# Kernel optimization log

Measured on AMD Instinct MI355X. Metric: run time of the kernel, lower is better.

## Reference

```python
import jax, jax.numpy as jnp
import numpy as np

BIN_SIZE = 128  # bin_size init arg

def elu(x):
    return jnp.where(x > 0, x, jnp.expm1(x))

def setup_inputs() -> dict:
    key = jax.random.key(0)
    ks = jax.random.split(key, 8)
    B, N, D, F = 2, 6400, 32, 256
    x_dist = jax.random.normal(ks[0], (B, N, D), jnp.float32)
    x_features = jax.random.normal(ks[1], (B, N, F), jnp.float32)
    msk = jax.random.randint(ks[2], (B, N), 0, 2) > 0
    codebook = jax.random.normal(ks[3], (D, 100), jnp.float32)  # (distance_dim, max_num_bins//2)
    W1 = jax.random.normal(ks[4], (2 * D, 32), jnp.float32) * (1.0 / np.sqrt(2 * D)).astype(np.float32)
    b1 = jnp.zeros((32,), jnp.float32)
    W2 = jax.random.normal(ks[5], (32, 32), jnp.float32) * np.float32(1.0 / np.sqrt(32))
    b2 = jnp.zeros((32,), jnp.float32)
    W3 = jax.random.normal(ks[6], (32, 32), jnp.float32) * np.float32(1.0 / np.sqrt(32))
    b3 = jnp.zeros((32,), jnp.float32)
    return dict(x_dist=x_dist, x_features=x_features, msk=msk, codebook=codebook,
                W1=W1, b1=b1, W2=W2, b2=b2, W3=W3, b3=b3)

def reference(x_dist, x_features, msk, codebook, W1, b1, W2, b2, W3, b3):
    B, N, D = x_dist.shape
    n_bins = N // BIN_SIZE
    # LSH projections: [B,N,n_bins//2] -> mirrored to [B,N,n_bins]
    mul = jnp.einsum('bnd,dh->bnh', x_dist, codebook[:, :n_bins // 2])
    cmul = jnp.concatenate([mul, -mul], axis=-1)
    # masked-out points are pushed into the last bin
    bin_idx = jnp.argmax(cmul, axis=-1) + jnp.where(~msk, n_bins - 1, 0)
    bins_split = jnp.argsort(bin_idx, axis=-1).reshape(B, n_bins, BIN_SIZE)  # [B,nb,bs]
    gather = jax.vmap(lambda x, i: x[i])  # batched gather over axis 1
    x_dist_binned = gather(x_dist, bins_split)          # [B,nb,bs,D]
    x_features_binned = gather(x_features, bins_split)  # [B,nb,bs,F]
    msk_f = msk.astype(x_dist.dtype)[..., None]         # [B,N,1]
    msk_f_binned = gather(msk_f, bins_split)            # [B,nb,bs,1]
    # pairwise learnable kernel: concat(a_i, b_j) -> 3-layer FFN -> elu
    a = jnp.broadcast_to(x_dist_binned[:, :, :, None, :], (B, n_bins, BIN_SIZE, BIN_SIZE, D))
    b = jnp.broadcast_to(x_dist_binned[:, :, None, :, :], (B, n_bins, BIN_SIZE, BIN_SIZE, D))
    res = jnp.concatenate([a, b], axis=-1)              # [B,nb,bs,bs,2D]
    h = elu(res @ W1 + b1)
    h = elu(h @ W2 + b2)
    dm = elu(h @ W3 + b3)                               # [B,nb,bs,bs,32]
    m = msk_f_binned[..., 0]                            # [B,nb,bs]
    dm = dm * m[:, :, :, None, None] * m[:, :, None, :, None]
    return (bins_split, x_features_binned, dm, msk_f_binned)
```

## Files before the change

kernel.cpp:

```cpp
#include <hip/hip_runtime.h>

#define BATCH 2
#define NPT 6400
#define DD 32
#define FF 256
#define BS 128
#define NBINS 50
#define NHALF 25
#define NPTS (BATCH * NPT)
#define NKEY 100
#define IST 8

typedef __bf16 bf16x8 __attribute__((ext_vector_type(8)));
typedef float f32x4 __attribute__((ext_vector_type(4)));

__device__ __forceinline__ float elu_f(float x) {
    return x > 0.0f ? x : (__expf(x) - 1.0f);
}

__global__ void k_binkey(const float* __restrict__ xd, const float* __restrict__ cb,
                         const int* __restrict__ msk, int* __restrict__ keys) {
    int g = blockIdx.x * blockDim.x + threadIdx.x;
    if (g >= NPTS) return;
    const float* xr = xd + (size_t)g * DD;
    float x[DD];
#pragma unroll
    for (int d = 0; d < DD; ++d) x[d] = xr[d];
    float mul[NHALF];
#pragma unroll
    for (int h = 0; h < NHALF; ++h) {
        float s = 0.f;
#pragma unroll
        for (int d = 0; d < DD; ++d) s = fmaf(x[d], cb[d * 100 + h], s);
        mul[h] = s;
    }
    float best = mul[0];
    int bi = 0;
#pragma unroll
    for (int h = 1; h < NHALF; ++h)
        if (mul[h] > best) { best = mul[h]; bi = h; }
#pragma unroll
    for (int h = 0; h < NHALF; ++h) {
        float v = -mul[h];
        if (v > best) { best = v; bi = NHALF + h; }
    }
    keys[g] = bi + (msk[g] != 0 ? 0 : (NBINS - 1));
}

__global__ void k_sort(const int* __restrict__ keys, float* __restrict__ bins_f,
                       int* __restrict__ bins_i) {
    __shared__ unsigned char sk[NPT];
    __shared__ unsigned short lh[NKEY][258];
    __shared__ int base[128];
    int b = blockIdx.x;
    int t = threadIdx.x;
    for (int i = t; i < NPT; i += 256) sk[i] = (unsigned char)keys[b * NPT + i];
    for (int k = 0; k < NKEY; ++k) lh[k][t] = 0;
    __syncthreads();
    const int CH = NPT / 256;
    int i0 = t * CH;
#pragma unroll
    for (int i = 0; i < CH; ++i) lh[sk[i0 + i]][t]++;
    __syncthreads();
    int myrun = 0;
    if (t < NKEY) {
        int run = 0;
        for (int c = 0; c < 256; ++c) {
            int v = lh[t][c];
            lh[t][c] = (unsigned short)run;
            run += v;
        }
        myrun = run;
    }
    if (t < 128) base[t] = myrun;
    __syncthreads();
    for (int off = 1; off < 128; off <<= 1) {
        int v = (t < 128 && t >= off) ? base[t - off] : 0;
        __syncthreads();
        if (t < 128) base[t] += v;
        __syncthreads();
    }
    if (t < 128) base[t] -= myrun;
    __syncthreads();
#pragma unroll
    for (int i = 0; i < CH; ++i) {
        int idx = i0 + i;
        int k = sk[idx];
        int pos = base[k] + lh[k][t];
        lh[k][t] = (unsigned short)(lh[k][t] + 1);
        bins_f[b * NPT + pos] = (float)idx;
        bins_i[b * NPT + pos] = idx;
    }
}

__global__ void k_points(const float* __restrict__ xd, const int* __restrict__ msk,
                         const int* __restrict__ bins_i, const float* __restrict__ W1,
                         const float* __restrict__ b1, float* __restrict__ a1b1,
                         float* __restrict__ mws, float* __restrict__ out_msk) {
    int g = blockIdx.x * blockDim.x + threadIdx.x;
    int p_lin = g >> 5;
    int c = g & 31;
    if (p_lin >= NPTS) return;
    int bb = p_lin / NPT;
    int idx = bins_i[p_lin];
    const float* xr = xd + ((size_t)(bb * NPT + idx)) * DD;
    float a = 0.f, bv = b1[c];
#pragma unroll
    for (int d = 0; d < DD; ++d) {
        float xv = xr[d];
        a = fmaf(xv, W1[d * 32 + c], a);
        bv = fmaf(xv, W1[(DD + d) * 32 + c], bv);
    }
    a1b1[(size_t)p_lin * 64 + c] = a;
    a1b1[(size_t)p_lin * 64 + 32 + c] = bv;
    if (c == 0) {
        float m = (msk[bb * NPT + idx] != 0) ? 1.0f : 0.0f;
        mws[p_lin] = m;
        out_msk[p_lin] = m;
    }
}

__global__ void k_feat(const float* __restrict__ xf, const int* __restrict__ bins_i,
                       float* __restrict__ out_feat) {
    int g = blockIdx.x * blockDim.x + threadIdx.x;
    if (g >= NPTS * (FF / 4)) return;
    int row = g >> 6;
    int q = g & 63;
    int bb = row / NPT;
    int idx = bins_i[row];
    const float4* src = (const float4*)(xf + ((size_t)(bb * NPT + idx)) * FF);
    float4* dst = (float4*)(out_feat + (size_t)row * FF);
    dst[q] = src[q];
}

__global__ void __launch_bounds__(256) k_pairs(
    const float* __restrict__ a1b1, const float* __restrict__ mws,
    const float* __restrict__ W2, const float* __restrict__ b2,
    const float* __restrict__ W3, const float* __restrict__ b3,
    float* __restrict__ out_dm) {
    __shared__ __attribute__((aligned(16))) float B1s[128][36];
    __shared__ __attribute__((aligned(16))) float A1s[IST][36];
    __shared__ float mjs[128];
    __shared__ float mis[IST];
    __shared__ __attribute__((aligned(16))) __bf16 scr[4][2][16 * 40];

    int t = threadIdx.x;
    int lane = t & 63;
    int wv = t >> 6;
    int n = lane & 15;
    int quad = lane >> 4;
    int koct = quad * 8;

    int bin = blockIdx.x >> 4;
    int strip = blockIdx.x & 15;
    int i_base = strip * IST;
    int base_p = bin * 128;

    for (int idx = t; idx < 128 * 8; idx += 256) {
        int r = idx >> 3, q = idx & 7;
        *(float4*)&B1s[r][q * 4] =
            *(const float4*)&a1b1[(size_t)(base_p + r) * 64 + 32 + q * 4];
    }
    if (t < IST * 8) {
        int r = t >> 3, q = t & 7;
        *(float4*)&A1s[r][q * 4] =
            *(const float4*)&a1b1[(size_t)(base_p + i_base + r) * 64 + q * 4];
    }
    if (t < 128) mjs[t] = mws[base_p + t];
    if (t < IST) mis[t] = mws[base_p + i_base + t];

    bf16x8 w2f0, w2f1, w3f0, w3f1;
#pragma unroll
    for (int j = 0; j < 8; ++j) {
        w2f0[j] = (__bf16)W2[(koct + j) * 32 + n];
        w2f1[j] = (__bf16)W2[(koct + j) * 32 + n + 16];
        w3f0[j] = (__bf16)W3[(koct + j) * 32 + n];
        w3f1[j] = (__bf16)W3[(koct + j) * 32 + n + 16];
    }
    float b2lo = b2[n], b2hi = b2[n + 16];
    float b3lo = b3[n], b3hi = b3[n + 16];
    __syncthreads();

    const f32x4 z = {0.f, 0.f, 0.f, 0.f};
    for (int g = 0; g < 16; ++g) {
        int grp = g * 4 + wv;
        int i_l = grp >> 3;
        int j0 = (grp & 7) * 16;

        float aA[8], bB[8];
        *(float4*)&aA[0] = *(float4*)&A1s[i_l][koct];
        *(float4*)&aA[4] = *(float4*)&A1s[i_l][koct + 4];
        *(float4*)&bB[0] = *(float4*)&B1s[j0 + n][koct];
        *(float4*)&bB[4] = *(float4*)&B1s[j0 + n][koct + 4];
        bf16x8 h1;
#pragma unroll
        for (int j = 0; j < 8; ++j) h1[j] = (__bf16)elu_f(aA[j] + bB[j]);

        f32x4 acc0 = __builtin_amdgcn_mfma_f32_16x16x32_bf16(h1, w2f0, z, 0, 0, 0);
        f32x4 acc1 = __builtin_amdgcn_mfma_f32_16x16x32_bf16(h1, w2f1, z, 0, 0, 0);

        __bf16* sc = &scr[wv][g & 1][0];
#pragma unroll
        for (int r = 0; r < 4; ++r) {
            sc[(quad * 4 + r) * 40 + n] = (__bf16)elu_f(acc0[r] + b2lo);
            sc[(quad * 4 + r) * 40 + n + 16] = (__bf16)elu_f(acc1[r] + b2hi);
        }
        __syncthreads();

        bf16x8 h2 = *(bf16x8*)&sc[n * 40 + koct];
        f32x4 acc2 = __builtin_amdgcn_mfma_f32_16x16x32_bf16(h2, w3f0, z, 0, 0, 0);
        f32x4 acc3 = __builtin_amdgcn_mfma_f32_16x16x32_bf16(h2, w3f1, z, 0, 0, 0);

        float miv = mis[i_l];
        size_t obase = ((size_t)(bin * 128 + i_base + i_l) * 128 + j0) * 32;
#pragma unroll
        for (int r = 0; r < 4; ++r) {
            int jr = quad * 4 + r;
            float mm = miv * mjs[j0 + jr];
            out_dm[obase + (size_t)jr * 32 + n] = elu_f(acc2[r] + b3lo) * mm;
            out_dm[obase + (size_t)jr * 32 + n + 16] = elu_f(acc3[r] + b3hi) * mm;
        }
    }
}

extern "C" void kernel_launch(void* const* d_in, const int* in_sizes, int n_in,
                              void* d_out, int out_size, void* d_ws, size_t ws_size,
                              hipStream_t stream) {
    const float* xd  = (const float*)d_in[0];
    const float* xf  = (const float*)d_in[1];
    const int*   msk = (const int*)d_in[2];
    const float* cb  = (const float*)d_in[3];
    const float* W1  = (const float*)d_in[4];
    const float* b1  = (const float*)d_in[5];
    const float* W2  = (const float*)d_in[6];
    const float* b2  = (const float*)d_in[7];
    const float* W3  = (const float*)d_in[8];
    const float* b3  = (const float*)d_in[9];

    float* out = (float*)d_out;
    float* out_bins = out;
    float* out_feat = out + 12800;
    float* out_dm   = out + 12800 + 3276800;
    float* out_msk  = out + 12800 + 3276800 + 52428800;

    int*   keys   = (int*)d_ws;
    int*   bins_i = keys + NPTS;
    float* a1b1   = (float*)(bins_i + NPTS);
    float* mws    = a1b1 + (size_t)NPTS * 64;

    k_binkey<<<NPTS / 256, 256, 0, stream>>>(xd, cb, msk, keys);
    k_sort<<<BATCH, 256, 0, stream>>>(keys, out_bins, bins_i);
    k_points<<<NPTS * 32 / 256, 256, 0, stream>>>(xd, msk, bins_i, W1, b1, a1b1, mws, out_msk);
    k_feat<<<NPTS * 64 / 256, 256, 0, stream>>>(xf, bins_i, out_feat);
    k_pairs<<<100 * 16, 256, 0, stream>>>(a1b1, mws, W2, b2, W3, b3, out_dm);
}
```

Before: 289.9 us.

## Fuse point gather kernels and drop block barrier in pair MLP loop

Merges the W1 projection kernel and the feature gather kernel into one launch, where each wavefront handles one point, copying its feature row and computing both halves of the first-layer projection. In the pair kernel, the per-iteration block-wide __syncthreads is removed and the double-buffered per-wave scratch becomes a single buffer. The scratch is private to each wave, so the barrier was not needed for data sharing. Dropping it relies on lockstep wavefront execution to order the LDS writes before the reads, with no explicit wave-level fence.

```diff
diff --git a/kernel.cpp b/kernel.cpp
--- a/kernel.cpp
+++ b/kernel.cpp
@@ -93,44 +93,39 @@
     }
 }
 
-__global__ void k_points(const float* __restrict__ xd, const int* __restrict__ msk,
-                         const int* __restrict__ bins_i, const float* __restrict__ W1,
-                         const float* __restrict__ b1, float* __restrict__ a1b1,
-                         float* __restrict__ mws, float* __restrict__ out_msk) {
-    int g = blockIdx.x * blockDim.x + threadIdx.x;
-    int p_lin = g >> 5;
-    int c = g & 31;
+__global__ void __launch_bounds__(256) k_gather(
+    const float* __restrict__ xd, const float* __restrict__ xf,
+    const int* __restrict__ msk, const int* __restrict__ bins_i,
+    const float* __restrict__ W1, const float* __restrict__ b1,
+    float* __restrict__ out_feat, float* __restrict__ a1b1,
+    float* __restrict__ mws, float* __restrict__ out_msk) {
+    int t = threadIdx.x;
+    int wv = t >> 6;
+    int l = t & 63;
+    int p_lin = blockIdx.x * 4 + wv;
     if (p_lin >= NPTS) return;
     int bb = p_lin / NPT;
     int idx = bins_i[p_lin];
-    const float* xr = xd + ((size_t)(bb * NPT + idx)) * DD;
-    float a = 0.f, bv = b1[c];
-#pragma unroll
-    for (int d = 0; d < DD; ++d) {
-        float xv = xr[d];
-        a = fmaf(xv, W1[d * 32 + c], a);
-        bv = fmaf(xv, W1[(DD + d) * 32 + c], bv);
-    }
-    a1b1[(size_t)p_lin * 64 + c] = a;
-    a1b1[(size_t)p_lin * 64 + 32 + c] = bv;
-    if (c == 0) {
-        float m = (msk[bb * NPT + idx] != 0) ? 1.0f : 0.0f;
+    int src_row = bb * NPT + idx;
+
+    const float4* src = (const float4*)(xf + (size_t)src_row * FF);
+    float4* dst = (float4*)(out_feat + (size_t)p_lin * FF);
+    dst[l] = src[l];
+
+    const float* xr = xd + (size_t)src_row * DD;
+    int c = l & 31;
+    int side = l >> 5;
+    float acc = side ? b1[c] : 0.f;
+    const float* Wcol = W1 + (size_t)side * DD * 32;
+#pragma unroll
+    for (int d = 0; d < DD; ++d) acc = fmaf(xr[d], Wcol[d * 32 + c], acc);
+    a1b1[(size_t)p_lin * 64 + l] = acc;
+
+    if (l == 0) {
+        float m = (msk[src_row] != 0) ? 1.0f : 0.0f;
         mws[p_lin] = m;
         out_msk[p_lin] = m;
     }
-}
-
-__global__ void k_feat(const float* __restrict__ xf, const int* __restrict__ bins_i,
-                       float* __restrict__ out_feat) {
-    int g = blockIdx.x * blockDim.x + threadIdx.x;
-    if (g >= NPTS * (FF / 4)) return;
-    int row = g >> 6;
-    int q = g & 63;
-    int bb = row / NPT;
-    int idx = bins_i[row];
-    const float4* src = (const float4*)(xf + ((size_t)(bb * NPT + idx)) * FF);
-    float4* dst = (float4*)(out_feat + (size_t)row * FF);
-    dst[q] = src[q];
 }
 
 __global__ void __launch_bounds__(256) k_pairs(
@@ -142,7 +137,7 @@
     __shared__ __attribute__((aligned(16))) float A1s[IST][36];
     __shared__ float mjs[128];
     __shared__ float mis[IST];
-    __shared__ __attribute__((aligned(16))) __bf16 scr[4][2][16 * 40];
+    __shared__ __attribute__((aligned(16))) __bf16 scr[4][16 * 40];
 
     int t = threadIdx.x;
     int lane = t & 63;
@@ -182,6 +177,7 @@
     __syncthreads();
 
     const f32x4 z = {0.f, 0.f, 0.f, 0.f};
+    __bf16* sc = &scr[wv][0];
     for (int g = 0; g < 16; ++g) {
         int grp = g * 4 + wv;
         int i_l = grp >> 3;
@@ -199,14 +195,11 @@
         f32x4 acc0 = __builtin_amdgcn_mfma_f32_16x16x32_bf16(h1, w2f0, z, 0, 0, 0);
         f32x4 acc1 = __builtin_amdgcn_mfma_f32_16x16x32_bf16(h1, w2f1, z, 0, 0, 0);
 
-        __bf16* sc = &scr[wv][g & 1][0];
 #pragma unroll
         for (int r = 0; r < 4; ++r) {
             sc[(quad * 4 + r) * 40 + n] = (__bf16)elu_f(acc0[r] + b2lo);
             sc[(quad * 4 + r) * 40 + n + 16] = (__bf16)elu_f(acc1[r] + b2hi);
         }
-        __syncthreads();
-
         bf16x8 h2 = *(bf16x8*)&sc[n * 40 + koct];
         f32x4 acc2 = __builtin_amdgcn_mfma_f32_16x16x32_bf16(h2, w3f0, z, 0, 0, 0);
         f32x4 acc3 = __builtin_amdgcn_mfma_f32_16x16x32_bf16(h2, w3f1, z, 0, 0, 0);
@@ -250,7 +243,7 @@
 
     k_binkey<<<NPTS / 256, 256, 0, stream>>>(xd, cb, msk, keys);
     k_sort<<<BATCH, 256, 0, stream>>>(keys, out_bins, bins_i);
-    k_points<<<NPTS * 32 / 256, 256, 0, stream>>>(xd, msk, bins_i, W1, b1, a1b1, mws, out_msk);
-    k_feat<<<NPTS * 64 / 256, 256, 0, stream>>>(xf, bins_i, out_feat);
+    k_gather<<<NPTS / 4, 256, 0, stream>>>(xd, xf, msk, bins_i, W1, b1,
+                                           out_feat, a1b1, mws, out_msk);
     k_pairs<<<100 * 16, 256, 0, stream>>>(a1b1, mws, W2, b2, W3, b3, out_dm);
 }
```

Measured after the change: 286.9 us. No clear change (-1.0%).
